# Optimization experiments

Hardware: AMD Instinct MI355X
Metric: run time of the kernel (lower is better)

Reference implementation:

```python
import jax, jax.numpy as jnp
import numpy as np

HEADS = 8
DIM_HEAD = 64
ROPE_BASE = 10000.0


def _rope_rotate(t):
    """lucidrains-style interleaved RoPE on t: [B, H, N, D]."""
    n, d = t.shape[-2], t.shape[-1]
    inv_freq = 1.0 / (ROPE_BASE ** (jnp.arange(0, d, 2, dtype=jnp.float32) / d))  # [D/2]
    freqs = jnp.arange(n, dtype=jnp.float32)[:, None] * inv_freq[None, :]          # [N, D/2]
    freqs = jnp.repeat(freqs, 2, axis=-1)                                           # [N, D], interleaved
    cos = jnp.cos(freqs).astype(t.dtype)
    sin = jnp.sin(freqs).astype(t.dtype)
    # rotate_half with interleaved pairs: (x1, x2) -> (-x2, x1)
    t2 = t.reshape(t.shape[:-1] + (d // 2, 2))
    rot = jnp.stack([-t2[..., 1], t2[..., 0]], axis=-1).reshape(t.shape)
    return t * cos + rot * sin


def setup_inputs() -> dict:
    key = jax.random.key(0)
    k1, k2, k3, k4 = jax.random.split(key, 4)
    B, N, DIM = 8, 1024, 512
    hidden = HEADS * DIM_HEAD  # 512
    x = jax.random.normal(k1, (B, N, DIM), dtype=jnp.float32)
    pos_bias = jax.random.normal(k2, (HEADS, N, N), dtype=jnp.float32) * 0.1
    w_qkv = jax.random.normal(k3, (DIM, hidden * 3), dtype=jnp.float32) * (DIM ** -0.5)
    w_out = jax.random.normal(k4, (hidden, DIM), dtype=jnp.float32) * (hidden ** -0.5)
    return {"x": x, "pos_bias": pos_bias, "w_qkv": w_qkv, "w_out": w_out}


def reference(x, pos_bias, w_qkv, w_out):
    B, N, _ = x.shape
    qkv = x @ w_qkv                                   # [B, N, 3*H*D]
    q, k, v = jnp.split(qkv, 3, axis=-1)

    def split_heads(t):
        return t.reshape(B, N, HEADS, DIM_HEAD).transpose(0, 2, 1, 3)  # [B, H, N, D]

    q, k, v = map(split_heads, (q, k, v))
    q = q * (DIM_HEAD ** -0.5)
    q = _rope_rotate(q)
    k = _rope_rotate(k)
    sim = jnp.einsum('bhid,bhjd->bhij', q, k) + pos_bias  # pos_bias [H,N,N] broadcasts over B
    attn = jax.nn.softmax(sim, axis=-1)                    # max-subtracted softmax (stable)
    out = jnp.einsum('bhij,bhjd->bhid', attn, v)
    out = out.transpose(0, 2, 1, 3).reshape(B, N, HEADS * DIM_HEAD)
    return out @ w_out
```

## Files before the change

kernel.cpp:

```cpp
#include <hip/hip_runtime.h>

#define DEV __device__ __forceinline__

typedef __attribute__((ext_vector_type(8))) short bf16x8;
typedef __attribute__((ext_vector_type(4))) short bf16x4;
typedef __attribute__((ext_vector_type(4))) float f32x4;
typedef __attribute__((ext_vector_type(4))) unsigned int u32x4;

constexpr int Bb = 8;
constexpr int Nn = 1024;
constexpr int DIMm = 512;
constexpr int Hh = 8;
constexpr int Dh = 64;
constexpr int Mm = Bb * Nn;
constexpr float LN10K = 9.210340371976184f;
constexpr float LOG2E = 1.4426950408889634f;

DEV short f2bf(float f) {
  unsigned int u = __float_as_uint(f);
  u += 0x7fffu + ((u >> 16) & 1u);
  return (short)(u >> 16);
}

DEV unsigned int cvtpk(float lo, float hi) {
  unsigned int r;
  asm("v_cvt_pk_bf16_f32 %0, %1, %2" : "=v"(r) : "v"(lo), "v"(hi));
  return r;
}

DEV bf16x8 comb(bf16x4 lo, bf16x4 hi) {
  bf16x8 r;
  r[0] = lo[0]; r[1] = lo[1]; r[2] = lo[2]; r[3] = lo[3];
  r[4] = hi[0]; r[5] = hi[1]; r[6] = hi[2]; r[7] = hi[3];
  return r;
}

DEV f32x4 mfma16(bf16x8 a, bf16x8 b, f32x4 c) {
  return __builtin_amdgcn_mfma_f32_16x16x32_bf16(a, b, c, 0, 0, 0);
}

__global__ void prep_kernel(const float* __restrict__ x, const float* __restrict__ wq,
                            const float* __restrict__ wo, short* __restrict__ x_bf,
                            short* __restrict__ wqkvT, short* __restrict__ woutT,
                            float2* __restrict__ tab) {
  int stride = gridDim.x * blockDim.x;
  int t = blockIdx.x * blockDim.x + threadIdx.x;
  for (int i = t; i < Mm * DIMm / 4; i += stride) {
    float4 v = ((const float4*)x)[i];
    bf16x4 o;
    o[0] = f2bf(v.x); o[1] = f2bf(v.y); o[2] = f2bf(v.z); o[3] = f2bf(v.w);
    *(bf16x4*)(x_bf + (size_t)i * 4) = o;
  }
  for (int i = t; i < 1536 * 512; i += stride) {
    int n = i >> 9, k = i & 511;
    wqkvT[i] = f2bf(wq[(size_t)k * 1536 + n]);
  }
  for (int i = t; i < 512 * 512; i += stride) {
    int n = i >> 9, k = i & 511;
    woutT[i] = f2bf(wo[(size_t)k * 512 + n]);
  }
  for (int i = t; i < Nn * 32; i += stride) {
    int n = i >> 5, d2 = i & 31;
    float fr = (float)n * __expf(-(float)(2 * d2) * (LN10K / 64.f));
    float sn, cs;
    __sincosf(fr, &sn, &cs);
    tab[i] = make_float2(cs, sn);
  }
}

template <int QKV>
__global__ __launch_bounds__(256) void gemm_k(const short* __restrict__ A,
                                              const short* __restrict__ Bt,
                                              float* __restrict__ outF,
                                              short* __restrict__ qr,
                                              short* __restrict__ kr,
                                              short* __restrict__ vt,
                                              const float2* __restrict__ tab) {
  __shared__ short Al[128][40];
  __shared__ short Bl[128][40];
  const int tid = threadIdx.x;
  const int lane = tid & 63;
  const int wid = tid >> 6;
  const int wm = wid >> 1, wn = wid & 1;
  const int li = lane & 15, g4 = (lane >> 4) << 2;
  const int m0 = blockIdx.x * 128, n0 = blockIdx.y * 128;

  f32x4 zero4 = {0.f, 0.f, 0.f, 0.f};
  f32x4 acc[4][4];
#pragma unroll
  for (int i = 0; i < 4; ++i)
#pragma unroll
    for (int j = 0; j < 4; ++j) acc[i][j] = zero4;

  for (int kt = 0; kt < 512; kt += 32) {
#pragma unroll
    for (int p = 0; p < 2; ++p) {
      int e = (tid + p * 256) * 8;
      int r = e >> 5, c = e & 31;
      *(u32x4*)(&Al[r][c]) = *(const u32x4*)(A + (size_t)(m0 + r) * 512 + kt + c);
      *(u32x4*)(&Bl[r][c]) = *(const u32x4*)(Bt + (size_t)(n0 + r) * 512 + kt + c);
    }
    __syncthreads();
    bf16x8 af[4], bfr[4];
#pragma unroll
    for (int mt = 0; mt < 4; ++mt) {
      int row = wm * 64 + mt * 16 + li;
      af[mt] = comb(*(const bf16x4*)(&Al[row][g4]), *(const bf16x4*)(&Al[row][16 + g4]));
    }
#pragma unroll
    for (int nt = 0; nt < 4; ++nt) {
      int row = wn * 64 + nt * 16 + li;
      bfr[nt] = comb(*(const bf16x4*)(&Bl[row][g4]), *(const bf16x4*)(&Bl[row][16 + g4]));
    }
#pragma unroll
    for (int mt = 0; mt < 4; ++mt)
#pragma unroll
      for (int nt = 0; nt < 4; ++nt)
        acc[mt][nt] = mfma16(af[mt], bfr[nt], acc[mt][nt]);
    __syncthreads();
  }

  if (QKV == 0) {
#pragma unroll
    for (int mt = 0; mt < 4; ++mt) {
      int mb = m0 + wm * 64 + mt * 16 + g4;
#pragma unroll
      for (int nt = 0; nt < 4; ++nt) {
        int c = n0 + wn * 64 + nt * 16 + li;
#pragma unroll
        for (int r = 0; r < 4; ++r) outF[(size_t)(mb + r) * 512 + c] = acc[mt][nt][r];
      }
    }
  } else {
    const int sec = n0 >> 9;
#pragma unroll
    for (int mt = 0; mt < 4; ++mt) {
      int mb = m0 + wm * 64 + mt * 16 + g4;
      int b_ = mb >> 10;
      int nb = mb & 1023;
#pragma unroll
      for (int nt = 0; nt < 4; ++nt) {
        int c = n0 + wn * 64 + nt * 16 + li;
        int cs = c & 511;
        int hh = cs >> 6, d = cs & 63;
        size_t bhoff = (size_t)(b_ * Hh + hh) * 65536;
        if (sec == 2) {
          int dt = d >> 4, liD = d & 15;
          int kkJ = (nb >> 5) & 1;
          int gj = (nb & 15) >> 2;
          int s0 = (nb & 16) >> 2;
          size_t off = bhoff + (size_t)(nb >> 6) * 4096 +
                       (size_t)((dt * 2 + kkJ) * 512) + (size_t)(liD + 16 * gj) * 8 + s0;
          uint2 st;
          st.x = cvtpk(acc[mt][nt][0], acc[mt][nt][1]);
          st.y = cvtpk(acc[mt][nt][2], acc[mt][nt][3]);
          *(uint2*)(vt + off) = st;
        } else {
          int kkD = d >> 5;
          int gd = (d & 15) >> 2;
          int sD = (d & 3) | ((d & 16) >> 2);
          size_t off = bhoff + (size_t)(nb >> 4) * 1024 + (size_t)(kkD * 512) +
                       (size_t)((nb & 15) + 16 * gd) * 8 + sD;
          short* dst = (sec == 0 ? qr : kr) + off;
#pragma unroll
          for (int r = 0; r < 4; ++r) {
            float v0 = acc[mt][nt][r];
            float vp = __shfl_xor(v0, 1, 64);
            float2 cssn = tab[(size_t)(nb + r) * 32 + (d >> 1)];
            float rot = (d & 1) ? vp : -vp;
            float res = v0 * cssn.x + rot * cssn.y;
            if (sec == 0) res *= 0.125f;
            dst[(size_t)r * 8] = f2bf(res);
          }
        }
      }
    }
  }
}

__global__ __launch_bounds__(256, 4) void attn_k(const short* __restrict__ qf_g,
                                                 const short* __restrict__ kf_g,
                                                 const short* __restrict__ vf_g,
                                                 const float* __restrict__ bias,
                                                 short* __restrict__ ao) {
  const int tid = threadIdx.x, lane = tid & 63, w = tid >> 6;
  const int li = lane & 15, g4 = (lane >> 4) << 2;
  const int bid = blockIdx.x;
  const int h = bid & 7;
  const int inner = bid >> 3;
  const int b_ = inner >> 4, it = inner & 15;
  const int bh = b_ * 8 + h;
  const int i0 = it * 64;
  const int iq = i0 + w * 16 + li;

  const short* qbase = qf_g + (size_t)bh * 65536 + (size_t)(it * 4 + w) * 1024 + lane * 8;
  bf16x8 qf0 = *(const bf16x8*)(qbase);
  bf16x8 qf1 = *(const bf16x8*)(qbase + 512);

  const short* kt = kf_g + (size_t)bh * 65536 + (size_t)lane * 8;
  const short* vtp = vf_g + (size_t)bh * 65536 + (size_t)lane * 8;
  const float* brow = bias + ((size_t)h * Nn + iq) * Nn + g4;

  float m_run = -1e30f, l_run = 0.f;
  f32x4 zero4 = {0.f, 0.f, 0.f, 0.f};
  f32x4 acc[4];
#pragma unroll
  for (int i = 0; i < 4; ++i) acc[i] = zero4;

  for (int t = 0; t < 16; ++t) {
    f32x4 bb[4];
#pragma unroll
    for (int js = 0; js < 4; ++js) bb[js] = *(const f32x4*)(brow + js * 16);
    brow += 64;

    bf16x8 kf[8];
#pragma unroll
    for (int i = 0; i < 4; ++i) kf[i] = *(const bf16x8*)(kt + i * 512);
#pragma unroll
    for (int i = 4; i < 8; ++i) kf[i] = *(const bf16x8*)(kt + 2048 + (i - 4) * 512);
    kt += 4096;

    f32x4 s[4];
    __builtin_amdgcn_s_setprio(1);
#pragma unroll
    for (int js = 0; js < 4; ++js) {
      f32x4 sa = mfma16(kf[js * 2], qf0, bb[js]);
      s[js] = mfma16(kf[js * 2 + 1], qf1, sa);
    }
    __builtin_amdgcn_s_setprio(0);

    float mx = fmaxf(fmaxf(fmaxf(s[0][0], s[0][1]), fmaxf(s[0][2], s[0][3])),
                     fmaxf(fmaxf(s[1][0], s[1][1]), fmaxf(s[1][2], s[1][3])));
    float mx2 = fmaxf(fmaxf(fmaxf(s[2][0], s[2][1]), fmaxf(s[2][2], s[2][3])),
                      fmaxf(fmaxf(s[3][0], s[3][1]), fmaxf(s[3][2], s[3][3])));
    mx = fmaxf(mx, mx2);
    mx = fmaxf(mx, __shfl_xor(mx, 16, 64));
    mx = fmaxf(mx, __shfl_xor(mx, 32, 64));

    bf16x8 vf[8];
#pragma unroll
    for (int i = 0; i < 4; ++i) vf[i] = *(const bf16x8*)(vtp + i * 512);
#pragma unroll
    for (int i = 4; i < 8; ++i) vf[i] = *(const bf16x8*)(vtp + 2048 + (i - 4) * 512);
    vtp += 4096;

    if (!__all(mx - m_run <= 8.0f)) {
      float mn = fmaxf(m_run, mx);
      float sc = __builtin_amdgcn_exp2f((m_run - mn) * LOG2E);
      l_run *= sc;
      m_run = mn;
      float fs0 = __shfl(sc, g4 + 0, 64), fs1 = __shfl(sc, g4 + 1, 64);
      float fs2 = __shfl(sc, g4 + 2, 64), fs3 = __shfl(sc, g4 + 3, 64);
#pragma unroll
      for (int dt = 0; dt < 4; ++dt) {
        acc[dt][0] *= fs0; acc[dt][1] *= fs1;
        acc[dt][2] *= fs2; acc[dt][3] *= fs3;
      }
    }

    float nm = -m_run * LOG2E;
    float rs = 0.f;
#pragma unroll
    for (int js = 0; js < 4; ++js)
#pragma unroll
      for (int r = 0; r < 4; ++r) {
        float p = __builtin_amdgcn_exp2f(__builtin_fmaf(s[js][r], LOG2E, nm));
        s[js][r] = p;
        rs += p;
      }
    rs += __shfl_xor(rs, 16, 64);
    rs += __shfl_xor(rs, 32, 64);
    l_run += rs;

    bf16x8 pf[2];
#pragma unroll
    for (int kk = 0; kk < 2; ++kk) {
      union { bf16x8 v; unsigned int d[4]; } u;
      u.d[0] = cvtpk(s[2 * kk][0], s[2 * kk][1]);
      u.d[1] = cvtpk(s[2 * kk][2], s[2 * kk][3]);
      u.d[2] = cvtpk(s[2 * kk + 1][0], s[2 * kk + 1][1]);
      u.d[3] = cvtpk(s[2 * kk + 1][2], s[2 * kk + 1][3]);
      pf[kk] = u.v;
    }

    __builtin_amdgcn_s_setprio(1);
#pragma unroll
    for (int dt = 0; dt < 4; ++dt) {
      f32x4 a = mfma16(pf[0], vf[dt * 2], acc[dt]);
      acc[dt] = mfma16(pf[1], vf[dt * 2 + 1], a);
    }
    __builtin_amdgcn_s_setprio(0);
  }

  float rl = 1.f / l_run;
  float fr0 = __shfl(rl, g4 + 0, 64), fr1 = __shfl(rl, g4 + 1, 64);
  float fr2 = __shfl(rl, g4 + 2, 64), fr3 = __shfl(rl, g4 + 3, 64);
#pragma unroll
  for (int dt = 0; dt < 4; ++dt) {
    float fr[4] = {fr0, fr1, fr2, fr3};
#pragma unroll
    for (int r = 0; r < 4; ++r) {
      int i_ = i0 + w * 16 + g4 + r;
      ao[((size_t)(b_ * Nn + i_)) * 512 + h * 64 + dt * 16 + li] =
          f2bf(acc[dt][r] * fr[r]);
    }
  }
}

extern "C" void kernel_launch(void* const* d_in, const int* in_sizes, int n_in,
                              void* d_out, int out_size, void* d_ws, size_t ws_size,
                              hipStream_t stream) {
  const float* x = (const float*)d_in[0];
  const float* pb = (const float*)d_in[1];
  const float* wq = (const float*)d_in[2];
  const float* wo = (const float*)d_in[3];
  float* out = (float*)d_out;

  short* w = (short*)d_ws;
  short* x_bf = w;  w += (size_t)Mm * DIMm;
  short* wqkvT = w; w += 1536 * 512;
  short* woutT = w; w += 512 * 512;
  short* qr = w;    w += (size_t)Mm * DIMm;
  short* kr = w;    w += (size_t)Mm * DIMm;
  short* vt = w;    w += (size_t)Mm * DIMm;
  float2* tab = (float2*)w; w += Nn * 32 * 4;
  short* ao = x_bf;

  prep_kernel<<<1024, 256, 0, stream>>>(x, wq, wo, x_bf, wqkvT, woutT, tab);
  gemm_k<1><<<dim3(64, 12), 256, 0, stream>>>(x_bf, wqkvT, nullptr, qr, kr, vt, tab);
  attn_k<<<1024, 256, 0, stream>>>(qr, kr, vt, pb, ao);
  gemm_k<0><<<dim3(64, 4), 256, 0, stream>>>(ao, woutT, out, nullptr, nullptr, nullptr, tab);
}
```

Measured before the change: 133.2 us.

## Software-pipeline attention loop with 32-key tiles and double-buffered K/bias prefetch

The attention inner loop now processes 32-key tiles instead of 64 and double-buffers the K fragments and bias loads, issuing the next tile's loads before computing the current one. Scheduling barriers keep the loads from being moved past the compute. The goal is to hide global memory latency behind the MFMA and softmax work and to reduce per-tile register pressure. In exchange, the online softmax max/rescale check and the shuffle reductions now run twice as often.

```diff
diff --git a/kernel.cpp b/kernel.cpp
--- a/kernel.cpp
+++ b/kernel.cpp
@@ -178,6 +178,82 @@
   }
 }
 
+struct KT {
+  bf16x8 k0, k1, k2, k3;
+  f32x4 b0, b1;
+};
+
+DEV void loadK(KT& T, const short* kb, const float* br, int t) {
+  const short* p = kb + (size_t)t * 2048;
+  T.k0 = *(const bf16x8*)(p);
+  T.k1 = *(const bf16x8*)(p + 512);
+  T.k2 = *(const bf16x8*)(p + 1024);
+  T.k3 = *(const bf16x8*)(p + 1536);
+  T.b0 = *(const f32x4*)(br + t * 32);
+  T.b1 = *(const f32x4*)(br + t * 32 + 16);
+}
+
+DEV void loadV(bf16x8* v, const short* vb, int t) {
+  const short* p = vb + (size_t)(t >> 1) * 4096 + (size_t)(t & 1) * 512;
+  v[0] = *(const bf16x8*)(p);
+  v[1] = *(const bf16x8*)(p + 1024);
+  v[2] = *(const bf16x8*)(p + 2048);
+  v[3] = *(const bf16x8*)(p + 3072);
+}
+
+DEV void tileC(const KT& T, const bf16x8* v, bf16x8 qf0, bf16x8 qf1,
+               f32x4* acc, float& m_run, float& l_run, int g4) {
+  __builtin_amdgcn_s_setprio(1);
+  f32x4 s0 = mfma16(T.k0, qf0, T.b0);
+  f32x4 s1 = mfma16(T.k2, qf0, T.b1);
+  s0 = mfma16(T.k1, qf1, s0);
+  s1 = mfma16(T.k3, qf1, s1);
+  __builtin_amdgcn_s_setprio(0);
+
+  float mx = fmaxf(fmaxf(fmaxf(s0[0], s0[1]), fmaxf(s0[2], s0[3])),
+                   fmaxf(fmaxf(s1[0], s1[1]), fmaxf(s1[2], s1[3])));
+  mx = fmaxf(mx, __shfl_xor(mx, 16, 64));
+  mx = fmaxf(mx, __shfl_xor(mx, 32, 64));
+
+  if (!__all(mx - m_run <= 8.0f)) {
+    float mn = fmaxf(m_run, mx);
+    float sc = __builtin_amdgcn_exp2f((m_run - mn) * LOG2E);
+    l_run *= sc;
+    m_run = mn;
+    float fs0 = __shfl(sc, g4 + 0, 64), fs1 = __shfl(sc, g4 + 1, 64);
+    float fs2 = __shfl(sc, g4 + 2, 64), fs3 = __shfl(sc, g4 + 3, 64);
+#pragma unroll
+    for (int dt = 0; dt < 4; ++dt) {
+      acc[dt][0] *= fs0; acc[dt][1] *= fs1;
+      acc[dt][2] *= fs2; acc[dt][3] *= fs3;
+    }
+  }
+
+  float nm = -m_run * LOG2E;
+  float rs = 0.f;
+  float e0[4], e1[4];
+#pragma unroll
+  for (int r = 0; r < 4; ++r) {
+    e0[r] = __builtin_amdgcn_exp2f(__builtin_fmaf(s0[r], LOG2E, nm));
+    e1[r] = __builtin_amdgcn_exp2f(__builtin_fmaf(s1[r], LOG2E, nm));
+    rs += e0[r] + e1[r];
+  }
+  rs += __shfl_xor(rs, 16, 64);
+  rs += __shfl_xor(rs, 32, 64);
+  l_run += rs;
+
+  union { bf16x8 v8; unsigned int d[4]; } u;
+  u.d[0] = cvtpk(e0[0], e0[1]);
+  u.d[1] = cvtpk(e0[2], e0[3]);
+  u.d[2] = cvtpk(e1[0], e1[1]);
+  u.d[3] = cvtpk(e1[2], e1[3]);
+
+  __builtin_amdgcn_s_setprio(1);
+#pragma unroll
+  for (int dt = 0; dt < 4; ++dt) acc[dt] = mfma16(u.v8, v[dt], acc[dt]);
+  __builtin_amdgcn_s_setprio(0);
+}
+
 __global__ __launch_bounds__(256, 4) void attn_k(const short* __restrict__ qf_g,
                                                  const short* __restrict__ kf_g,
                                                  const short* __restrict__ vf_g,
@@ -197,9 +273,9 @@
   bf16x8 qf0 = *(const bf16x8*)(qbase);
   bf16x8 qf1 = *(const bf16x8*)(qbase + 512);
 
-  const short* kt = kf_g + (size_t)bh * 65536 + (size_t)lane * 8;
-  const short* vtp = vf_g + (size_t)bh * 65536 + (size_t)lane * 8;
-  const float* brow = bias + ((size_t)h * Nn + iq) * Nn + g4;
+  const short* kb = kf_g + (size_t)bh * 65536 + (size_t)lane * 8;
+  const short* vb = vf_g + (size_t)bh * 65536 + (size_t)lane * 8;
+  const float* br = bias + ((size_t)h * Nn + iq) * Nn + g4;
 
   float m_run = -1e30f, l_run = 0.f;
   f32x4 zero4 = {0.f, 0.f, 0.f, 0.f};
@@ -207,89 +283,21 @@
 #pragma unroll
   for (int i = 0; i < 4; ++i) acc[i] = zero4;
 
-  for (int t = 0; t < 16; ++t) {
-    f32x4 bb[4];
-#pragma unroll
-    for (int js = 0; js < 4; ++js) bb[js] = *(const f32x4*)(brow + js * 16);
-    brow += 64;
-
-    bf16x8 kf[8];
-#pragma unroll
-    for (int i = 0; i < 4; ++i) kf[i] = *(const bf16x8*)(kt + i * 512);
-#pragma unroll
-    for (int i = 4; i < 8; ++i) kf[i] = *(const bf16x8*)(kt + 2048 + (i - 4) * 512);
-    kt += 4096;
-
-    f32x4 s[4];
-    __builtin_amdgcn_s_setprio(1);
-#pragma unroll
-    for (int js = 0; js < 4; ++js) {
-      f32x4 sa = mfma16(kf[js * 2], qf0, bb[js]);
-      s[js] = mfma16(kf[js * 2 + 1], qf1, sa);
-    }
-    __builtin_amdgcn_s_setprio(0);
-
-    float mx = fmaxf(fmaxf(fmaxf(s[0][0], s[0][1]), fmaxf(s[0][2], s[0][3])),
-                     fmaxf(fmaxf(s[1][0], s[1][1]), fmaxf(s[1][2], s[1][3])));
-    float mx2 = fmaxf(fmaxf(fmaxf(s[2][0], s[2][1]), fmaxf(s[2][2], s[2][3])),
-                      fmaxf(fmaxf(s[3][0], s[3][1]), fmaxf(s[3][2], s[3][3])));
-    mx = fmaxf(mx, mx2);
-    mx = fmaxf(mx, __shfl_xor(mx, 16, 64));
-    mx = fmaxf(mx, __shfl_xor(mx, 32, 64));
-
-    bf16x8 vf[8];
-#pragma unroll
-    for (int i = 0; i < 4; ++i) vf[i] = *(const bf16x8*)(vtp + i * 512);
-#pragma unroll
-    for (int i = 4; i < 8; ++i) vf[i] = *(const bf16x8*)(vtp + 2048 + (i - 4) * 512);
-    vtp += 4096;
-
-    if (!__all(mx - m_run <= 8.0f)) {
-      float mn = fmaxf(m_run, mx);
-      float sc = __builtin_amdgcn_exp2f((m_run - mn) * LOG2E);
-      l_run *= sc;
-      m_run = mn;
-      float fs0 = __shfl(sc, g4 + 0, 64), fs1 = __shfl(sc, g4 + 1, 64);
-      float fs2 = __shfl(sc, g4 + 2, 64), fs3 = __shfl(sc, g4 + 3, 64);
-#pragma unroll
-      for (int dt = 0; dt < 4; ++dt) {
-        acc[dt][0] *= fs0; acc[dt][1] *= fs1;
-        acc[dt][2] *= fs2; acc[dt][3] *= fs3;
-      }
-    }
-
-    float nm = -m_run * LOG2E;
-    float rs = 0.f;
-#pragma unroll
-    for (int js = 0; js < 4; ++js)
-#pragma unroll
-      for (int r = 0; r < 4; ++r) {
-        float p = __builtin_amdgcn_exp2f(__builtin_fmaf(s[js][r], LOG2E, nm));
-        s[js][r] = p;
-        rs += p;
-      }
-    rs += __shfl_xor(rs, 16, 64);
-    rs += __shfl_xor(rs, 32, 64);
-    l_run += rs;
-
-    bf16x8 pf[2];
-#pragma unroll
-    for (int kk = 0; kk < 2; ++kk) {
-      union { bf16x8 v; unsigned int d[4]; } u;
-      u.d[0] = cvtpk(s[2 * kk][0], s[2 * kk][1]);
-      u.d[1] = cvtpk(s[2 * kk][2], s[2 * kk][3]);
-      u.d[2] = cvtpk(s[2 * kk + 1][0], s[2 * kk + 1][1]);
-      u.d[3] = cvtpk(s[2 * kk + 1][2], s[2 * kk + 1][3]);
-      pf[kk] = u.v;
-    }
-
-    __builtin_amdgcn_s_setprio(1);
-#pragma unroll
-    for (int dt = 0; dt < 4; ++dt) {
-      f32x4 a = mfma16(pf[0], vf[dt * 2], acc[dt]);
-      acc[dt] = mfma16(pf[1], vf[dt * 2 + 1], a);
-    }
-    __builtin_amdgcn_s_setprio(0);
+  KT tA, tB;
+  bf16x8 vr[4];
+  loadK(tA, kb, br, 0);
+
+#pragma unroll 1
+  for (int t = 0; t < 32; t += 2) {
+    loadK(tB, kb, br, t + 1);
+    loadV(vr, vb, t);
+    __builtin_amdgcn_sched_barrier(0x38F);
+    tileC(tA, vr, qf0, qf1, acc, m_run, l_run, g4);
+
+    if (t + 2 < 32) loadK(tA, kb, br, t + 2);
+    loadV(vr, vb, t + 1);
+    __builtin_amdgcn_sched_barrier(0x38F);
+    tileC(tB, vr, qf0, qf1, acc, m_run, l_run, g4);
   }
 
   float rl = 1.f / l_run;
```

Result: no change. 132.0 us (-0.9%).

## Stage K/V tiles in double-buffered LDS via direct global-to-LDS loads

Applied to the files above, without the earlier changes.

The attention kernel now copies each 64-row K and V tile once per block into a double-buffered shared-memory slot using global_load_lds. The four waves then read their MFMA operands from LDS instead of each wave loading the same tiles from global memory. The next tile and its bias values are prefetched while the current tile is computed, with a wait and barrier at the end of each iteration. The block index mapping also changes so that neighbouring blocks share a query tile and head across batches, which should improve L2 reuse of the position bias. The cost is 32 KB of LDS per block and a block-wide barrier on every tile.

```diff
diff --git a/kernel.cpp b/kernel.cpp
--- a/kernel.cpp
+++ b/kernel.cpp
@@ -37,6 +37,12 @@
 
 DEV f32x4 mfma16(bf16x8 a, bf16x8 b, f32x4 c) {
   return __builtin_amdgcn_mfma_f32_16x16x32_bf16(a, b, c, 0, 0, 0);
+}
+
+DEV void gload16(const void* g, void* l) {
+  __builtin_amdgcn_global_load_lds(
+      (const __attribute__((address_space(1))) void*)g,
+      (__attribute__((address_space(3))) void*)l, 16, 0, 0);
 }
 
 __global__ void prep_kernel(const float* __restrict__ x, const float* __restrict__ wq,
@@ -178,17 +184,22 @@
   }
 }
 
+constexpr int KVB = 64;
+constexpr int NTT = Nn / KVB;
+
 __global__ __launch_bounds__(256, 4) void attn_k(const short* __restrict__ qf_g,
                                                  const short* __restrict__ kf_g,
                                                  const short* __restrict__ vf_g,
                                                  const float* __restrict__ bias,
                                                  short* __restrict__ ao) {
+  __shared__ short Kls[2][4096];
+  __shared__ short Vls[2][4096];
   const int tid = threadIdx.x, lane = tid & 63, w = tid >> 6;
   const int li = lane & 15, g4 = (lane >> 4) << 2;
   const int bid = blockIdx.x;
   const int h = bid & 7;
-  const int inner = bid >> 3;
-  const int b_ = inner >> 4, it = inner & 15;
+  const int b_ = (bid >> 3) & 7;
+  const int it = bid >> 6;
   const int bh = b_ * 8 + h;
   const int i0 = it * 64;
   const int iq = i0 + w * 16 + li;
@@ -197,9 +208,9 @@
   bf16x8 qf0 = *(const bf16x8*)(qbase);
   bf16x8 qf1 = *(const bf16x8*)(qbase + 512);
 
-  const short* kt = kf_g + (size_t)bh * 65536 + (size_t)lane * 8;
-  const short* vtp = vf_g + (size_t)bh * 65536 + (size_t)lane * 8;
-  const float* brow = bias + ((size_t)h * Nn + iq) * Nn + g4;
+  const short* kb = kf_g + (size_t)bh * 65536;
+  const short* vb = vf_g + (size_t)bh * 65536;
+  const float* br = bias + ((size_t)h * Nn + iq) * Nn + g4;
 
   float m_run = -1e30f, l_run = 0.f;
   f32x4 zero4 = {0.f, 0.f, 0.f, 0.f};
@@ -207,25 +218,46 @@
 #pragma unroll
   for (int i = 0; i < 4; ++i) acc[i] = zero4;
 
-  for (int t = 0; t < 16; ++t) {
-    f32x4 bb[4];
-#pragma unroll
-    for (int js = 0; js < 4; ++js) bb[js] = *(const f32x4*)(brow + js * 16);
-    brow += 64;
-
-    bf16x8 kf[8];
-#pragma unroll
-    for (int i = 0; i < 4; ++i) kf[i] = *(const bf16x8*)(kt + i * 512);
-#pragma unroll
-    for (int i = 4; i < 8; ++i) kf[i] = *(const bf16x8*)(kt + 2048 + (i - 4) * 512);
-    kt += 4096;
-
+#define STAGE_TILE(T, BUF)                                                  \
+  do {                                                                      \
+    const short* ks_ = kb + (size_t)(T) * 4096;                             \
+    const short* vs_ = vb + (size_t)(T) * 4096;                             \
+    gload16(ks_ + (size_t)tid * 8, &Kls[BUF][(size_t)(w * 64) * 8]);        \
+    gload16(ks_ + (size_t)(256 + tid) * 8,                                  \
+            &Kls[BUF][(size_t)(256 + w * 64) * 8]);                         \
+    gload16(vs_ + (size_t)tid * 8, &Vls[BUF][(size_t)(w * 64) * 8]);        \
+    gload16(vs_ + (size_t)(256 + tid) * 8,                                  \
+            &Vls[BUF][(size_t)(256 + w * 64) * 8]);                         \
+  } while (0)
+
+  f32x4 bbA[4], bbB[4];
+
+  STAGE_TILE(0, 0);
+#pragma unroll
+  for (int js = 0; js < 4; ++js) bbA[js] = *(const f32x4*)(br + js * 16);
+  asm volatile("s_waitcnt vmcnt(0)" ::: "memory");
+  __builtin_amdgcn_s_barrier();
+
+  int cur = 0;
+#pragma unroll 1
+  for (int t = 0; t < NTT; ++t) {
+    if (t + 1 < NTT) {
+      STAGE_TILE(t + 1, cur ^ 1);
+#pragma unroll
+      for (int js = 0; js < 4; ++js)
+        bbB[js] = *(const f32x4*)(br + (t + 1) * 64 + js * 16);
+    }
+
+    const short* KB = &Kls[cur][0];
+    const short* VB = &Vls[cur][0];
     f32x4 s[4];
     __builtin_amdgcn_s_setprio(1);
 #pragma unroll
     for (int js = 0; js < 4; ++js) {
-      f32x4 sa = mfma16(kf[js * 2], qf0, bb[js]);
-      s[js] = mfma16(kf[js * 2 + 1], qf1, sa);
+      bf16x8 k0 = *(const bf16x8*)(KB + js * 1024 + lane * 8);
+      bf16x8 k1 = *(const bf16x8*)(KB + js * 1024 + 512 + lane * 8);
+      f32x4 sa = mfma16(k0, qf0, bbA[js]);
+      s[js] = mfma16(k1, qf1, sa);
     }
     __builtin_amdgcn_s_setprio(0);
 
@@ -236,13 +268,6 @@
     mx = fmaxf(mx, mx2);
     mx = fmaxf(mx, __shfl_xor(mx, 16, 64));
     mx = fmaxf(mx, __shfl_xor(mx, 32, 64));
-
-    bf16x8 vf[8];
-#pragma unroll
-    for (int i = 0; i < 4; ++i) vf[i] = *(const bf16x8*)(vtp + i * 512);
-#pragma unroll
-    for (int i = 4; i < 8; ++i) vf[i] = *(const bf16x8*)(vtp + 2048 + (i - 4) * 512);
-    vtp += 4096;
 
     if (!__all(mx - m_run <= 8.0f)) {
       float mn = fmaxf(m_run, mx);
@@ -275,22 +300,31 @@
     bf16x8 pf[2];
 #pragma unroll
     for (int kk = 0; kk < 2; ++kk) {
-      union { bf16x8 v; unsigned int d[4]; } u;
+      union { bf16x8 v8; unsigned int d[4]; } u;
       u.d[0] = cvtpk(s[2 * kk][0], s[2 * kk][1]);
       u.d[1] = cvtpk(s[2 * kk][2], s[2 * kk][3]);
       u.d[2] = cvtpk(s[2 * kk + 1][0], s[2 * kk + 1][1]);
       u.d[3] = cvtpk(s[2 * kk + 1][2], s[2 * kk + 1][3]);
-      pf[kk] = u.v;
+      pf[kk] = u.v8;
     }
 
     __builtin_amdgcn_s_setprio(1);
 #pragma unroll
     for (int dt = 0; dt < 4; ++dt) {
-      f32x4 a = mfma16(pf[0], vf[dt * 2], acc[dt]);
-      acc[dt] = mfma16(pf[1], vf[dt * 2 + 1], a);
+      bf16x8 vf0 = *(const bf16x8*)(VB + (dt * 2 + 0) * 512 + lane * 8);
+      bf16x8 vf1 = *(const bf16x8*)(VB + (dt * 2 + 1) * 512 + lane * 8);
+      f32x4 a = mfma16(pf[0], vf0, acc[dt]);
+      acc[dt] = mfma16(pf[1], vf1, a);
     }
     __builtin_amdgcn_s_setprio(0);
-  }
+
+    asm volatile("s_waitcnt vmcnt(0)" ::: "memory");
+    __builtin_amdgcn_s_barrier();
+#pragma unroll
+    for (int js = 0; js < 4; ++js) bbA[js] = bbB[js];
+    cur ^= 1;
+  }
+#undef STAGE_TILE
 
   float rl = 1.f / l_run;
   float fr0 = __shfl(rl, g4 + 0, 64), fr1 = __shfl(rl, g4 + 1, 64);
```

Result: faster. 117.6 us (-11.7%).
